# Kernel tuning notes

Hardware: AMD Instinct MI355X
Metric: run time of the kernel (lower is better)

## Reference

```python
import jax, jax.numpy as jnp
import numpy as np

E = 768      # embed_dim (hidden_size)
H = 12       # num_attention_heads
DH = E // H  # head_dim = 64
B, S = 8, 1024


def setup_inputs() -> dict:
    key = jax.random.key(0)
    ks = jax.random.split(key, 10)
    sc = 1.0 / np.sqrt(E)
    inp = {
        "hidden_state": jax.random.normal(ks[0], (B, S, E), dtype=jnp.float32),
        # per-head Q/K/V projections, stacked over heads: [H, E, DH]
        "Wq": jax.random.normal(ks[1], (H, E, DH), dtype=jnp.float32) * sc,
        "bq": jax.random.normal(ks[2], (H, DH), dtype=jnp.float32) * 0.02,
        "Wk": jax.random.normal(ks[3], (H, E, DH), dtype=jnp.float32) * sc,
        "bk": jax.random.normal(ks[4], (H, DH), dtype=jnp.float32) * 0.02,
        "Wv": jax.random.normal(ks[5], (H, E, DH), dtype=jnp.float32) * sc,
        "bv": jax.random.normal(ks[6], (H, DH), dtype=jnp.float32) * 0.02,
        # output projection: [E, E]
        "Wo": jax.random.normal(ks[7], (E, E), dtype=jnp.float32) * sc,
        "bo": jax.random.normal(ks[8], (E,), dtype=jnp.float32) * 0.02,
    }
    return inp


def reference(hidden_state, Wq, bq, Wk, bk, Wv, bv, Wo, bo):
    # Q/K/V per head: [B,S,E] x [H,E,D] -> [B,H,S,D]
    q = jnp.einsum("bse,hed->bhsd", hidden_state, Wq) + bq[None, :, None, :]
    k = jnp.einsum("bse,hed->bhsd", hidden_state, Wk) + bk[None, :, None, :]
    v = jnp.einsum("bse,hed->bhsd", hidden_state, Wv) + bv[None, :, None, :]
    scale = 1.0 / jnp.sqrt(jnp.asarray(DH, dtype=q.dtype))
    scores = jnp.einsum("bhsd,bhtd->bhst", q, k) * scale   # [B,H,S,S]
    weights = jax.nn.softmax(scores, axis=-1)
    attn = jnp.einsum("bhst,bhtd->bhsd", weights, v)        # [B,H,S,D]
    # concat heads (head order matches ModuleList concat): [B,S,H*D]=[B,S,E]
    x = attn.transpose(0, 2, 1, 3).reshape(hidden_state.shape[0], hidden_state.shape[1], E)
    return x @ Wo + bo
```

## Files before the change

### kernel.cpp

```cpp
#include <hip/hip_runtime.h>

typedef unsigned short u16;
typedef __bf16 bf16;
typedef bf16 bf16x8 __attribute__((ext_vector_type(8)));
typedef float f32x4 __attribute__((ext_vector_type(4)));
typedef u16 u16x4 __attribute__((ext_vector_type(4)));
typedef u16 u16x8 __attribute__((ext_vector_type(8)));

#define MROWS 8192
#define EDIM 768
#define NQKV 2304
#define NHEAD 12
#define DH 64
#define SEQ 1024
#define BATCH 8
#define BH 96
#define BHSD (BH * SEQ * DH)
#define KIT64 (EDIM / 64)

#if __has_builtin(__builtin_amdgcn_exp2f)
#define EXP2(x) __builtin_amdgcn_exp2f(x)
#else
#define EXP2(x) exp2f(x)
#endif

__device__ __forceinline__ u16 f2bf(float f) {
  bf16 b = (bf16)f;
  return __builtin_bit_cast(u16, b);
}

__device__ __forceinline__ void gload_lds16(const u16* g, u16* l) {
  __builtin_amdgcn_global_load_lds(
      (const __attribute__((address_space(1))) void*)g,
      (__attribute__((address_space(3))) void*)l, 16, 0, 0);
}


__global__ void cvt_x(const float* __restrict__ x, u16* __restrict__ xb, int n) {
  int i = (blockIdx.x * blockDim.x + threadIdx.x) * 4;
  if (i >= n) return;
  float4 v = *(const float4*)(x + i);
  u16x4 o;
  o[0] = f2bf(v.x); o[1] = f2bf(v.y); o[2] = f2bf(v.z); o[3] = f2bf(v.w);
  *(u16x4*)(xb + i) = o;
}

__global__ __launch_bounds__(256) void pack_w(
    const float* __restrict__ Wq, const float* __restrict__ Wk,
    const float* __restrict__ Wv, const float* __restrict__ Wo,
    u16* __restrict__ Wt, u16* __restrict__ Wot) {
  __shared__ float T[64][65];
  int bid = blockIdx.x;
  int tid = threadIdx.x;
  int c = tid & 63, r4 = tid >> 6;
  if (bid < 432) {
    int region = bid / 144, rem = bid - region * 144;
    int h = rem / 12, e0 = (rem - h * 12) * 64;
    const float* W = region == 0 ? Wq : (region == 1 ? Wk : Wv);
    for (int p = 0; p < 16; p++) {
      int er = r4 + p * 4;
      T[er][c] = W[(size_t)(h * EDIM + e0 + er) * DH + c];
    }
    __syncthreads();
    int nbase = region * EDIM + h * 64;
    for (int p = 0; p < 16; p++) {
      int dr = r4 + p * 4;
      Wt[(size_t)(nbase + dr) * EDIM + e0 + c] = f2bf(T[c][dr]);
    }
  } else {
    bid -= 432;
    int n0 = (bid / 12) * 64, e0 = (bid - (bid / 12) * 12) * 64;
    for (int p = 0; p < 16; p++) {
      int er = r4 + p * 4;
      T[er][c] = Wo[(size_t)(e0 + er) * EDIM + n0 + c];
    }
    __syncthreads();
    for (int p = 0; p < 16; p++) {
      int dr = r4 + p * 4;
      Wot[(size_t)(n0 + dr) * EDIM + e0 + c] = f2bf(T[c][dr]);
    }
  }
}

template <int BM, int BN, int NW>
__device__ __forceinline__ void gemm_core(
    const u16* __restrict__ A, const u16* __restrict__ Bt,
    u16* As, u16* Bs, int m0, int n0, int tid, f32x4 acc[4][4]) {
  constexpr int NT = NW * 64;
  constexpr int RPP = NT / 8;
  constexpr int AP = BM / RPP;
  constexpr int BP = BN / RPP;
  constexpr int WMN = BM / 64;
  int wv = __builtin_amdgcn_readfirstlane(tid >> 6);
  int lane = tid & 63, quad = lane >> 4, l16 = lane & 15;
  int wm = (wv % WMN) * 64, wn = (wv / WMN) * 64;
  int srow = tid >> 3, cpos = tid & 7;
  int swcol = (cpos ^ (srow & 7)) * 8;
  const u16* Ag = A + (size_t)(m0 + srow) * EDIM + swcol;
  const u16* Bg = Bt + (size_t)(n0 + srow) * EDIM + swcol;
  u16* Asl = As + srow * 64 + cpos * 8;
  u16* Bsl = Bs + srow * 64 + cpos * 8;

  for (int k = 0; k < KIT64; k++) {
    __syncthreads();
    const u16* ak = Ag + k * 64;
    const u16* bk = Bg + k * 64;
#pragma unroll
    for (int p = 0; p < AP; p++)
      gload_lds16(ak + (size_t)(p * RPP) * EDIM, Asl + p * RPP * 64);
#pragma unroll
    for (int p = 0; p < BP; p++)
      gload_lds16(bk + (size_t)(p * RPP) * EDIM, Bsl + p * RPP * 64);
    __syncthreads();
#pragma unroll
    for (int kh = 0; kh < 2; kh++) {
      bf16x8 af[4], bfr[4];
      for (int i = 0; i < 4; i++) {
        int row = wm + i * 16 + l16;
        af[i] = *(const bf16x8*)(As + row * 64 + (((kh * 4 + quad) ^ (row & 7))) * 8);
      }
      for (int j = 0; j < 4; j++) {
        int row = wn + j * 16 + l16;
        bfr[j] = *(const bf16x8*)(Bs + row * 64 + (((kh * 4 + quad) ^ (row & 7))) * 8);
      }
      for (int i = 0; i < 4; i++)
        for (int j = 0; j < 4; j++)
          acc[i][j] = __builtin_amdgcn_mfma_f32_16x16x32_bf16(af[i], bfr[j], acc[i][j], 0, 0, 0);
    }
  }
}

__global__ __launch_bounds__(512, 4) void gemm_qkv(
    const u16* __restrict__ A, const u16* __restrict__ Bt,
    const float* __restrict__ bq, const float* __restrict__ bk, const float* __restrict__ bv,
    u16* __restrict__ qkv) {
  __shared__ __align__(16) u16 As[256 * 64];
  __shared__ __align__(16) u16 Bs[128 * 64];
  int tid = threadIdx.x;
  int wv = tid >> 6, lane = tid & 63, quad = lane >> 4, l16 = lane & 15;
  int wm = (wv % 4) * 64, wn = (wv / 4) * 64;
  int lin = blockIdx.y * 32 + blockIdx.x;
  int xcd = lin & 7, r = lin >> 3;
  int m0 = (xcd * 4 + (r & 3)) * 256;
  int n0 = (r >> 2) * 128;
  f32x4 acc[4][4] = {};
  gemm_core<256, 128, 8>(A, Bt, As, Bs, m0, n0, tid, acc);

  const float kQscale = 0.18033688011112042f;
  for (int i = 0; i < 4; i++) {
    int row0 = m0 + wm + i * 16 + quad * 4;
    for (int j = 0; j < 4; j++) {
      int n = n0 + wn + j * 16 + l16;
      int region = n / EDIM;
      int hd = n - region * EDIM;
      int h = hd >> 6, d = hd & 63;
      const float* bp = region == 0 ? bq : (region == 1 ? bk : bv);
      float bias = bp[hd];
      float scale = region == 0 ? kQscale : 1.0f;
      for (int r4 = 0; r4 < 4; r4++) {
        int rr = row0 + r4;
        int bb = rr >> 10, s = rr & 1023;
        float val = (acc[i][j][r4] + bias) * scale;
        u16 bv16 = f2bf(val);
        int bhh = bb * NHEAD + h;
        if (region < 2) {
          qkv[(size_t)region * BHSD + ((size_t)bhh * SEQ + s) * DH + d] = bv16;
        } else {
          qkv[(size_t)2 * BHSD + ((size_t)bhh * DH + d) * SEQ + s] = bv16;
        }
      }
    }
  }
}

__global__ __launch_bounds__(256, 4) void attn_kernel(const u16* __restrict__ qkv, u16* __restrict__ attn) {
  int lin = blockIdx.y * 96 + blockIdx.x;
  int xcd = lin & 7, rr6 = lin >> 3;
  int bh = xcd * 12 + (rr6 >> 4);
  int qt = rr6 & 15;
  int b = bh / NHEAD, h = bh - b * NHEAD;
  const u16* Q  = qkv + (size_t)bh * SEQ * DH;
  const u16* K  = qkv + (size_t)(BH + bh) * SEQ * DH;
  const u16* VT = qkv + (size_t)(2 * BH + bh) * SEQ * DH;
  int tid = threadIdx.x, wave = tid >> 6, lane = tid & 63, quad = lane >> 4, l16 = lane & 15;
  int q_base = qt * 64 + wave * 16;

  __shared__ __align__(16) u16 Ks[2][64 * 64];
  __shared__ __align__(16) u16 Vts[2][64 * 64];
  __shared__ __align__(16) u16 Ps[4][16 * 64];

  bf16x8 qf[2];
  for (int c = 0; c < 2; c++)
    qf[c] = *(const bf16x8*)(Q + (size_t)(q_base + l16) * DH + c * 32 + quad * 8);

  f32x4 o[4] = {};
  float psum[4] = {};

  int tr = tid >> 3, cpos = tid & 7;
  int ssw = (cpos ^ (tr & 7)) * 8;
  const u16* Kg0 = K + (size_t)tr * DH + ssw;
  const u16* Kg1 = K + (size_t)(tr + 32) * DH + ssw;
  const u16* Vg0 = VT + (size_t)tr * SEQ + ssw;
  const u16* Vg1 = VT + (size_t)(tr + 32) * SEQ + ssw;
  int dst0 = tr * 64 + cpos * 8;
  int dst1 = (tr + 32) * 64 + cpos * 8;

  gload_lds16(Kg0, Ks[0] + dst0);
  gload_lds16(Kg1, Ks[0] + dst1);
  gload_lds16(Vg0, Vts[0] + dst0);
  gload_lds16(Vg1, Vts[0] + dst1);
  __syncthreads();

  int buf = 0;
  for (int t0 = 0; t0 < SEQ; t0 += 64) {
    if (t0 + 64 < SEQ) {
      int nb = buf ^ 1;
      gload_lds16(Kg0 + (size_t)(t0 + 64) * DH, Ks[nb] + dst0);
      gload_lds16(Kg1 + (size_t)(t0 + 64) * DH, Ks[nb] + dst1);
      gload_lds16(Vg0 + t0 + 64, Vts[nb] + dst0);
      gload_lds16(Vg1 + t0 + 64, Vts[nb] + dst1);
    }
    const u16* Kb = Ks[buf];
    const u16* Vb = Vts[buf];

    float p[4][4];
    __builtin_amdgcn_s_setprio(1);
    for (int tc = 0; tc < 4; tc++) {
      int krow = tc * 16 + l16, k7 = l16 & 7;
      bf16x8 kf0 = *(const bf16x8*)(Kb + krow * 64 + ((quad ^ k7) * 8));
      bf16x8 kf1 = *(const bf16x8*)(Kb + krow * 64 + (((4 + quad) ^ k7) * 8));
      f32x4 z = {};
      z = __builtin_amdgcn_mfma_f32_16x16x32_bf16(qf[0], kf0, z, 0, 0, 0);
      z = __builtin_amdgcn_mfma_f32_16x16x32_bf16(qf[1], kf1, z, 0, 0, 0);
      for (int r = 0; r < 4; r++) {
        p[tc][r] = EXP2(z[r]);
        psum[r] += p[tc][r];
      }
    }
    __builtin_amdgcn_s_setprio(0);

    u16* P = Ps[wave];
    for (int tc = 0; tc < 4; tc++)
      for (int r = 0; r < 4; r++) {
        int prow = quad * 4 + r;
        int pc = tc * 2 + (l16 >> 3);
        P[prow * 64 + ((pc ^ (prow & 7)) * 8) + (l16 & 7)] = f2bf(p[tc][r]);
      }
    bf16x8 pf[2];
    for (int kc = 0; kc < 2; kc++)
      pf[kc] = *(const bf16x8*)(Ps[wave] + l16 * 64 + (((kc * 4 + quad) ^ (l16 & 7)) * 8));

    __builtin_amdgcn_s_setprio(1);
    for (int n = 0; n < 4; n++) {
      int vrow = n * 16 + l16, v7 = l16 & 7;
      bf16x8 vf0 = *(const bf16x8*)(Vb + vrow * 64 + ((quad ^ v7) * 8));
      bf16x8 vf1 = *(const bf16x8*)(Vb + vrow * 64 + (((4 + quad) ^ v7) * 8));
      o[n] = __builtin_amdgcn_mfma_f32_16x16x32_bf16(pf[0], vf0, o[n], 0, 0, 0);
      o[n] = __builtin_amdgcn_mfma_f32_16x16x32_bf16(pf[1], vf1, o[n], 0, 0, 0);
    }
    __builtin_amdgcn_s_setprio(0);

    __syncthreads();
    buf ^= 1;
  }

  for (int m = 1; m < 16; m <<= 1)
    for (int r = 0; r < 4; r++)
      psum[r] += __shfl_xor(psum[r], m);

  for (int r = 0; r < 4; r++) {
    float inv = 1.0f / psum[r];
    int qrow = q_base + quad * 4 + r;
    size_t rowoff = (size_t)(b * SEQ + qrow) * EDIM + h * DH;
    for (int n = 0; n < 4; n++)
      attn[rowoff + n * 16 + l16] = f2bf(o[n][r] * inv);
  }
}

__global__ __launch_bounds__(128, 3) void gemm_out(
    const u16* __restrict__ A, const u16* __restrict__ Bt,
    const float* __restrict__ bo, float* __restrict__ out) {
  __shared__ __align__(16) u16 As[64 * 64];
  __shared__ __align__(16) u16 Bs[128 * 64];
  int tid = threadIdx.x;
  int wv = tid >> 6, lane = tid & 63, quad = lane >> 4, l16 = lane & 15;
  int wn = wv * 64;
  int lin = blockIdx.y * 128 + blockIdx.x;
  int xcd = lin & 7, r = lin >> 3;
  int m0 = (xcd * 16 + (r & 15)) * 64;
  int n0 = (r >> 4) * 128;
  f32x4 acc[4][4] = {};
  gemm_core<64, 128, 2>(A, Bt, As, Bs, m0, n0, tid, acc);

  for (int i = 0; i < 4; i++) {
    int row0 = m0 + i * 16 + quad * 4;
    for (int j = 0; j < 4; j++) {
      int n = n0 + wn + j * 16 + l16;
      float bias = bo[n];
      for (int r4 = 0; r4 < 4; r4++)
        out[(size_t)(row0 + r4) * EDIM + n] = acc[i][j][r4] + bias;
    }
  }
}

extern "C" void kernel_launch(void* const* d_in, const int* in_sizes, int n_in,
                              void* d_out, int out_size, void* d_ws, size_t ws_size,
                              hipStream_t stream) {
  const float* x  = (const float*)d_in[0];
  const float* Wq = (const float*)d_in[1];
  const float* bq = (const float*)d_in[2];
  const float* Wk = (const float*)d_in[3];
  const float* bk = (const float*)d_in[4];
  const float* Wv = (const float*)d_in[5];
  const float* bv = (const float*)d_in[6];
  const float* Wo = (const float*)d_in[7];
  const float* bo = (const float*)d_in[8];
  float* out = (float*)d_out;
  char* ws = (char*)d_ws;

  u16* Xb   = (u16*)(ws);
  u16* Wt   = (u16*)(ws + 12582912);
  u16* Wot  = (u16*)(ws + 16121856);
  u16* qkv  = (u16*)(ws + 17301504);
  u16* attn = (u16*)(ws + 55050240);

  cvt_x<<<6144, 256, 0, stream>>>(x, Xb, MROWS * EDIM);
  pack_w<<<576, 256, 0, stream>>>(Wq, Wk, Wv, Wo, Wt, Wot);
  gemm_qkv<<<dim3(32, 18), 512, 0, stream>>>(Xb, Wt, bq, bk, bv, qkv);
  attn_kernel<<<dim3(96, 16), 256, 0, stream>>>(qkv, attn);
  gemm_out<<<dim3(128, 6), 128, 0, stream>>>(attn, Wot, bo, out);
}
```

Measured before the change: 228.0 us.

## Process two query groups per wave in attention and shrink QKV GEMM tile

The attention kernel now gives each wave 32 query rows (two 16-row groups) instead of 16. Each K/V fragment read from LDS feeds twice as many MFMAs, and the grid halves to 768 blocks. Probabilities are written to LDS directly inside the QK loop rather than staged in registers first. Separately, the QKV GEMM moves from 256x128 tiles with 512 threads to 128x128 tiles with 256 threads, doubling its block count. The cost is higher register pressure in attention (occupancy hint lowered to 3) and fewer blocks to fill the GPU.

Result: faster. 200.7 us (-12.0%).

```diff
diff --git a/kernel.cpp b/kernel.cpp
--- a/kernel.cpp
+++ b/kernel.cpp
@@ -130,21 +130,21 @@
   }
 }
 
-__global__ __launch_bounds__(512, 4) void gemm_qkv(
+__global__ __launch_bounds__(256, 4) void gemm_qkv(
     const u16* __restrict__ A, const u16* __restrict__ Bt,
     const float* __restrict__ bq, const float* __restrict__ bk, const float* __restrict__ bv,
     u16* __restrict__ qkv) {
-  __shared__ __align__(16) u16 As[256 * 64];
+  __shared__ __align__(16) u16 As[128 * 64];
   __shared__ __align__(16) u16 Bs[128 * 64];
   int tid = threadIdx.x;
   int wv = tid >> 6, lane = tid & 63, quad = lane >> 4, l16 = lane & 15;
-  int wm = (wv % 4) * 64, wn = (wv / 4) * 64;
-  int lin = blockIdx.y * 32 + blockIdx.x;
-  int xcd = lin & 7, r = lin >> 3;
-  int m0 = (xcd * 4 + (r & 3)) * 256;
-  int n0 = (r >> 2) * 128;
+  int wm = (wv & 1) * 64, wn = (wv >> 1) * 64;
+  int lin = blockIdx.y * 64 + blockIdx.x;
+  int xcd = lin & 7, r8 = lin >> 3;
+  int m0 = (xcd * 8 + (r8 & 7)) * 128;
+  int n0 = (r8 >> 3) * 128;
   f32x4 acc[4][4] = {};
-  gemm_core<256, 128, 8>(A, Bt, As, Bs, m0, n0, tid, acc);
+  gemm_core<128, 128, 4>(A, Bt, As, Bs, m0, n0, tid, acc);
 
   const float kQscale = 0.18033688011112042f;
   for (int i = 0; i < 4; i++) {
@@ -173,28 +173,29 @@
   }
 }
 
-__global__ __launch_bounds__(256, 4) void attn_kernel(const u16* __restrict__ qkv, u16* __restrict__ attn) {
+__global__ __launch_bounds__(256, 3) void attn_kernel(const u16* __restrict__ qkv, u16* __restrict__ attn) {
   int lin = blockIdx.y * 96 + blockIdx.x;
-  int xcd = lin & 7, rr6 = lin >> 3;
-  int bh = xcd * 12 + (rr6 >> 4);
-  int qt = rr6 & 15;
+  int xcd = lin & 7, rr = lin >> 3;
+  int bh = xcd * 12 + (rr >> 3);
+  int qt = rr & 7;
   int b = bh / NHEAD, h = bh - b * NHEAD;
   const u16* Q  = qkv + (size_t)bh * SEQ * DH;
   const u16* K  = qkv + (size_t)(BH + bh) * SEQ * DH;
   const u16* VT = qkv + (size_t)(2 * BH + bh) * SEQ * DH;
   int tid = threadIdx.x, wave = tid >> 6, lane = tid & 63, quad = lane >> 4, l16 = lane & 15;
-  int q_base = qt * 64 + wave * 16;
+  int q_base = qt * 128 + wave * 32;
 
   __shared__ __align__(16) u16 Ks[2][64 * 64];
   __shared__ __align__(16) u16 Vts[2][64 * 64];
-  __shared__ __align__(16) u16 Ps[4][16 * 64];
-
-  bf16x8 qf[2];
-  for (int c = 0; c < 2; c++)
-    qf[c] = *(const bf16x8*)(Q + (size_t)(q_base + l16) * DH + c * 32 + quad * 8);
-
-  f32x4 o[4] = {};
-  float psum[4] = {};
+  __shared__ __align__(16) u16 Ps[4][32 * 64];
+
+  bf16x8 qf[2][2];
+  for (int g = 0; g < 2; g++)
+    for (int c = 0; c < 2; c++)
+      qf[g][c] = *(const bf16x8*)(Q + (size_t)(q_base + g * 16 + l16) * DH + c * 32 + quad * 8);
+
+  f32x4 o[2][4] = {};
+  float psum[2][4] = {};
 
   int tr = tid >> 3, cpos = tid & 7;
   int ssw = (cpos ^ (tr & 7)) * 8;
@@ -212,6 +213,7 @@
   __syncthreads();
 
   int buf = 0;
+  u16* P = Ps[wave];
   for (int t0 = 0; t0 < SEQ; t0 += 64) {
     if (t0 + 64 < SEQ) {
       int nb = buf ^ 1;
@@ -223,40 +225,40 @@
     const u16* Kb = Ks[buf];
     const u16* Vb = Vts[buf];
 
-    float p[4][4];
     __builtin_amdgcn_s_setprio(1);
     for (int tc = 0; tc < 4; tc++) {
       int krow = tc * 16 + l16, k7 = l16 & 7;
       bf16x8 kf0 = *(const bf16x8*)(Kb + krow * 64 + ((quad ^ k7) * 8));
       bf16x8 kf1 = *(const bf16x8*)(Kb + krow * 64 + (((4 + quad) ^ k7) * 8));
-      f32x4 z = {};
-      z = __builtin_amdgcn_mfma_f32_16x16x32_bf16(qf[0], kf0, z, 0, 0, 0);
-      z = __builtin_amdgcn_mfma_f32_16x16x32_bf16(qf[1], kf1, z, 0, 0, 0);
-      for (int r = 0; r < 4; r++) {
-        p[tc][r] = EXP2(z[r]);
-        psum[r] += p[tc][r];
+      int pc = tc * 2 + (l16 >> 3);
+      for (int g = 0; g < 2; g++) {
+        f32x4 z = {};
+        z = __builtin_amdgcn_mfma_f32_16x16x32_bf16(qf[g][0], kf0, z, 0, 0, 0);
+        z = __builtin_amdgcn_mfma_f32_16x16x32_bf16(qf[g][1], kf1, z, 0, 0, 0);
+        for (int r = 0; r < 4; r++) {
+          float pv = EXP2(z[r]);
+          psum[g][r] += pv;
+          int prow = g * 16 + quad * 4 + r;
+          P[prow * 64 + ((pc ^ (prow & 7)) * 8) + (l16 & 7)] = f2bf(pv);
+        }
       }
     }
     __builtin_amdgcn_s_setprio(0);
 
-    u16* P = Ps[wave];
-    for (int tc = 0; tc < 4; tc++)
-      for (int r = 0; r < 4; r++) {
-        int prow = quad * 4 + r;
-        int pc = tc * 2 + (l16 >> 3);
-        P[prow * 64 + ((pc ^ (prow & 7)) * 8) + (l16 & 7)] = f2bf(p[tc][r]);
-      }
-    bf16x8 pf[2];
-    for (int kc = 0; kc < 2; kc++)
-      pf[kc] = *(const bf16x8*)(Ps[wave] + l16 * 64 + (((kc * 4 + quad) ^ (l16 & 7)) * 8));
+    bf16x8 pf[2][2];
+    for (int g = 0; g < 2; g++)
+      for (int kc = 0; kc < 2; kc++)
+        pf[g][kc] = *(const bf16x8*)(P + (g * 16 + l16) * 64 + (((kc * 4 + quad) ^ (l16 & 7)) * 8));
 
     __builtin_amdgcn_s_setprio(1);
     for (int n = 0; n < 4; n++) {
       int vrow = n * 16 + l16, v7 = l16 & 7;
       bf16x8 vf0 = *(const bf16x8*)(Vb + vrow * 64 + ((quad ^ v7) * 8));
       bf16x8 vf1 = *(const bf16x8*)(Vb + vrow * 64 + (((4 + quad) ^ v7) * 8));
-      o[n] = __builtin_amdgcn_mfma_f32_16x16x32_bf16(pf[0], vf0, o[n], 0, 0, 0);
-      o[n] = __builtin_amdgcn_mfma_f32_16x16x32_bf16(pf[1], vf1, o[n], 0, 0, 0);
+      for (int g = 0; g < 2; g++) {
+        o[g][n] = __builtin_amdgcn_mfma_f32_16x16x32_bf16(pf[g][0], vf0, o[g][n], 0, 0, 0);
+        o[g][n] = __builtin_amdgcn_mfma_f32_16x16x32_bf16(pf[g][1], vf1, o[g][n], 0, 0, 0);
+      }
     }
     __builtin_amdgcn_s_setprio(0);
 
@@ -264,16 +266,17 @@
     buf ^= 1;
   }
 
-  for (int m = 1; m < 16; m <<= 1)
-    for (int r = 0; r < 4; r++)
-      psum[r] += __shfl_xor(psum[r], m);
-
-  for (int r = 0; r < 4; r++) {
-    float inv = 1.0f / psum[r];
-    int qrow = q_base + quad * 4 + r;
-    size_t rowoff = (size_t)(b * SEQ + qrow) * EDIM + h * DH;
-    for (int n = 0; n < 4; n++)
-      attn[rowoff + n * 16 + l16] = f2bf(o[n][r] * inv);
+  for (int g = 0; g < 2; g++) {
+    for (int m = 1; m < 16; m <<= 1)
+      for (int r = 0; r < 4; r++)
+        psum[g][r] += __shfl_xor(psum[g][r], m);
+    for (int r = 0; r < 4; r++) {
+      float inv = 1.0f / psum[g][r];
+      int qrow = q_base + g * 16 + quad * 4 + r;
+      size_t rowoff = (size_t)(b * SEQ + qrow) * EDIM + h * DH;
+      for (int n = 0; n < 4; n++)
+        attn[rowoff + n * 16 + l16] = f2bf(o[g][n][r] * inv);
+    }
   }
 }
 
@@ -326,7 +329,7 @@
 
   cvt_x<<<6144, 256, 0, stream>>>(x, Xb, MROWS * EDIM);
   pack_w<<<576, 256, 0, stream>>>(Wq, Wk, Wv, Wo, Wt, Wot);
-  gemm_qkv<<<dim3(32, 18), 512, 0, stream>>>(Xb, Wt, bq, bk, bv, qkv);
-  attn_kernel<<<dim3(96, 16), 256, 0, stream>>>(qkv, attn);
+  gemm_qkv<<<dim3(64, 18), 256, 0, stream>>>(Xb, Wt, bq, bk, bv, qkv);
+  attn_kernel<<<dim3(96, 8), 256, 0, stream>>>(qkv, attn);
   gemm_out<<<dim3(128, 6), 128, 0, stream>>>(attn, Wot, bo, out);
 }
```
